# Kernel tuning notes

Hardware: AMD Instinct MI355X
Metric: run time of the kernel (lower is better)

Reference implementation:

```python
import jax, jax.numpy as jnp
import numpy as np

B, S, D = 32, 512, 512          # batch, max splits, HIDDEN_SIZE
H2 = D // 2                      # bidirectional GRU hidden per direction = 256
HEADS = 8
ATT_H = 512                      # ML_ATT_HIDDEN
DK = ATT_H // HEADS
LN_EPS = 1e-5


def setup_inputs() -> dict:
    key = jax.random.key(0)
    ks = jax.random.split(key, 20)
    n = lambda k, shp, s=0.05: jax.random.normal(k, shp, dtype=jnp.float32) * s
    lengths = jax.random.randint(ks[0], (B,), 1, S + 1)
    masks = (jnp.arange(S)[None, :] < lengths[:, None]).astype(jnp.int32)
    return {
        "splits": n(ks[1], (B, S, D), 1.0),
        "w_ih_f": n(ks[2], (3 * H2, D)), "w_hh_f": n(ks[3], (3 * H2, H2)),
        "b_ih_f": n(ks[4], (3 * H2,)), "b_hh_f": n(ks[5], (3 * H2,)),
        "w_ih_b": n(ks[6], (3 * H2, D)), "w_hh_b": n(ks[7], (3 * H2, H2)),
        "b_ih_b": n(ks[8], (3 * H2,)), "b_hh_b": n(ks[9], (3 * H2,)),
        "ln1_g": jnp.ones((D,), jnp.float32), "ln1_b": jnp.zeros((D,), jnp.float32),
        "wq": n(ks[10], (ATT_H, D)), "bq": n(ks[11], (ATT_H,)),
        "wk": n(ks[12], (ATT_H, D)), "bk": n(ks[13], (ATT_H,)),
        "wv": n(ks[14], (ATT_H, D)), "bv": n(ks[15], (ATT_H,)),
        "wo": n(ks[16], (D, ATT_H)), "bo": n(ks[17], (D,)),
        "ln2_g": jnp.ones((D,), jnp.float32), "ln2_b": jnp.zeros((D,), jnp.float32),
        "lengths": lengths, "masks": masks,
    }


def _gru_dir(x, m, w_ih, w_hh, b_ih, b_hh):
    """x: (B,S,D) float, m: (B,S) float {0,1}. Masked GRU, packed-sequence semantics:
    hidden frozen past length, outputs zero at pads, returns (outputs (B,S,H2), h_final (B,H2))."""
    xg = jnp.einsum('bsd,gd->bsg', x, w_ih) + b_ih   # precompute input gates (B,S,3H2)
    xg_t = xg.transpose(1, 0, 2)                      # (S,B,3H2)
    m_t = m.T[:, :, None]                             # (S,B,1)
    h0 = jnp.zeros((x.shape[0], w_hh.shape[1]), x.dtype)

    def step(h, inp):
        xg_s, m_s = inp
        hg = h @ w_hh.T + b_hh
        xr, xz, xn = jnp.split(xg_s, 3, -1)
        hr, hz, hn = jnp.split(hg, 3, -1)
        r = jax.nn.sigmoid(xr + hr)
        z = jax.nn.sigmoid(xz + hz)
        ncand = jnp.tanh(xn + r * hn)
        h_new = (1.0 - z) * ncand + z * h
        h = m_s * h_new + (1.0 - m_s) * h
        return h, h * m_s

    hT, ys = jax.lax.scan(step, h0, (xg_t, m_t))
    return ys.transpose(1, 0, 2), hT


def _layernorm(x, g, b):
    mu = x.mean(-1, keepdims=True)
    var = ((x - mu) ** 2).mean(-1, keepdims=True)
    return (x - mu) / jnp.sqrt(var + LN_EPS) * g + b


def reference(splits, w_ih_f, w_hh_f, b_ih_f, b_hh_f, w_ih_b, w_hh_b, b_ih_b, b_hh_b,
              ln1_g, ln1_b, wq, bq, wk, bk, wv, bv, wo, bo, ln2_g, ln2_b,
              lengths, masks):
    mf = masks.astype(splits.dtype)  # (B,S)
    # bidirectional masked GRU (split_rnn)
    out_f, h_f = _gru_dir(splits, mf, w_ih_f, w_hh_f, b_ih_f, b_hh_f)
    out_b_rev, h_b = _gru_dir(splits[:, ::-1], mf[:, ::-1], w_ih_b, w_hh_b, b_ih_b, b_hh_b)
    outputs = jnp.concatenate([out_f, out_b_rev[:, ::-1]], -1)  # (B,S,D)
    hidden = jnp.concatenate([h_f, h_b], -1)                    # (B,D)
    zm = (lengths != 0).astype(outputs.dtype)
    outputs = outputs * zm[:, None, None]
    hidden = hidden * zm[:, None]
    # split_rnn_norm (LAYER_NORM_USE)
    outputs = _layernorm(outputs, ln1_g, ln1_b)
    # CONTEXT_ATT: masked multi-head self-attention
    m3 = mf[:, None, :] * mf[:, :, None]        # (B,S,S)
    bsz = outputs.shape[0]

    def proj(x, w, b):
        return (x @ w.T + b).reshape(bsz, -1, HEADS, DK).transpose(0, 2, 1, 3)

    q = proj(outputs, wq, bq)
    k = proj(outputs, wk, bk)
    v = proj(outputs, wv, bv)
    scores = jnp.einsum('bhqd,bhkd->bhqk', q, k) / np.sqrt(DK).astype(outputs.dtype)
    mask4 = m3[:, None, :, :]
    scores = jnp.where(mask4 == 0, jnp.asarray(-1e8, scores.dtype), scores)
    p = jax.nn.softmax(scores, axis=-1) * mask4
    attn = jnp.einsum('bhqk,bhkd->bhqd', p, v)
    concat = attn.transpose(0, 2, 1, 3).reshape(bsz, -1, HEADS * DK)
    o = concat @ wo.T + bo
    rowmask = (m3.sum(-1, keepdims=True) > 0).astype(o.dtype)   # (B,S,1)
    o = o * rowmask
    # residual + attn_norm
    outputs = _layernorm(outputs + o, ln2_g, ln2_b)
    return outputs, hidden
```

## Files before the change

kernel.cpp:

```cpp
#include <hip/hip_runtime.h>
#include <hip/hip_bf16.h>
#include <hip/hip_fp16.h>


typedef __bf16 bf16_t;
typedef _Float16 f16_t;
typedef __bf16 bf16x8 __attribute__((ext_vector_type(8)));
typedef __bf16 bf16x4 __attribute__((ext_vector_type(4)));
typedef _Float16 f16x8 __attribute__((ext_vector_type(8)));
typedef float f32x4 __attribute__((ext_vector_type(4)));

#define NB 32
#define NS 512
#define ND 512
#define NH 8
#define DKq 64
#define CH 16

static __device__ __forceinline__ float sigm(float x){ return 1.0f/(1.0f+__expf(-x)); }
static __device__ __forceinline__ float tanh_fast(float x){ return 1.0f - 2.0f/(__expf(2.0f*x)+1.0f); }

__global__ void cvt_f32_bf16_k(const float* __restrict__ src, bf16_t* __restrict__ dst, int n4){
    int i = blockIdx.x*256 + threadIdx.x;
    if (i < n4){
        float4 v = ((const float4*)src)[i];
        bf16x4 o; o[0]=(bf16_t)v.x; o[1]=(bf16_t)v.y; o[2]=(bf16_t)v.z; o[3]=(bf16_t)v.w;
        ((bf16x4*)dst)[i] = o;
    }
}

template<int MODE>
__global__ __launch_bounds__(256,2) void gemm_k(
    const bf16_t* __restrict__ A, const bf16_t* __restrict__ W,
    const float* __restrict__ bias, void* __restrict__ out, void* __restrict__ out2,
    const int* __restrict__ masks, int N)
{
    const int lane = threadIdx.x & 63;
    const int wv = threadIdx.x >> 6;
    const int wr = wv >> 1, wc = wv & 1;
    const int m0 = blockIdx.y*128 + wr*64;
    const int n0 = blockIdx.x*128 + wc*64;
    const int r16 = lane & 15, kq = lane >> 4;
    f32x4 acc[4][4] = {};
    const bf16_t* Ap = A + (size_t)(m0 + r16)*512 + kq*8;
    const bf16_t* Wp = W + (size_t)(n0 + r16)*512 + kq*8;
    #pragma unroll
    for (int kk = 0; kk < 16; ++kk){
        bf16x8 a[4], b[4];
        #pragma unroll
        for (int i=0;i<4;++i) a[i] = *(const bf16x8*)(Ap + (size_t)i*16*512 + kk*32);
        #pragma unroll
        for (int j=0;j<4;++j) b[j] = *(const bf16x8*)(Wp + (size_t)j*16*512 + kk*32);
        #pragma unroll
        for (int i=0;i<4;++i)
            #pragma unroll
            for (int j=0;j<4;++j)
                acc[i][j] = __builtin_amdgcn_mfma_f32_16x16x32_bf16(a[i], b[j], acc[i][j], 0,0,0);
    }
    #pragma unroll
    for (int i=0;i<4;++i){
        int row_base = m0 + i*16 + kq*4;
        #pragma unroll
        for (int j=0;j<4;++j){
            int col = n0 + j*16 + r16;
            float bs = bias[col];
            #pragma unroll
            for (int r=0;r<4;++r){
                int row = row_base + r;
                float v = acc[i][j][r] + bs;
                if (MODE==0){
                    if (col < 768) ((f16_t*)out)[(size_t)row*768 + col] = (f16_t)v;
                    else           ((f16_t*)out2)[(size_t)row*768 + (col-768)] = (f16_t)v;
                } else if (MODE==1){
                    int which = col >> 9, hh = (col >> 6) & 7, d = col & 63;
                    int bb = row >> 9, s = row & 511;
                    ((bf16_t*)out)[((((size_t)which*NB + bb)*NH + hh)*NS + s)*DKq + d] = (bf16_t)v;
                } else {
                    float mrow = (float)masks[row];
                    ((float*)out)[(size_t)row*N + col] = v * mrow;
                }
            }
        }
    }
}

__global__ __launch_bounds__(512,2) void gru_scan_k(
    const f16_t* __restrict__ xg_f, const f16_t* __restrict__ xg_b,
    const float* __restrict__ whh_f, const float* __restrict__ whh_b,
    const float* __restrict__ bhh_f, const float* __restrict__ bhh_b,
    const int* __restrict__ lengths,
    f16_t* __restrict__ gout,
    float* __restrict__ hidden)
{
    const int b = blockIdx.x >> 1, dir = blockIdx.x & 1;
    const int tid = threadIdx.x, lane = tid & 63, w = tid >> 6;
    const int r16 = lane & 15, kq = lane >> 4;
    const float* whh = dir ? whh_b : whh_f;
    const float* bhh = dir ? bhh_b : bhh_f;
    const f16_t* xgd = dir ? xg_b : xg_f;
    const int len = lengths[b];

    __shared__ __align__(16) f16_t  xg_lds[2][CH][768];
    __shared__ __align__(16) f16_t  go_lds[CH][256];
    __shared__ __align__(16) bf16_t h_row[2][256];

    ((bf16_t*)h_row)[tid] = (bf16_t)0.0f;

    const int t0 = dir ? (NS - len) : 0;
    const int t_end = dir ? NS : len;
    const int nch = (len + CH - 1) / CH;

    auto issue_chunk = [&](int ci, int buf){
        int base = t0 + ci*CH;
        int jmax = min(CH, t_end - base);
        int pstart = dir ? (NS - base - jmax) : base;
        const char* gp = (const char*)(xgd + ((size_t)b*NS + pstart)*768);
        char* lp = (char*)(&xg_lds[buf][0][0]);
        int bytes = jmax*1536;
        #pragma unroll
        for (int k2=0; k2<3; ++k2){
            int off = (w*3 + k2)*1024;
            if (off < bytes){
                __builtin_amdgcn_global_load_lds(
                    (const __attribute__((address_space(1))) void*)(gp + off + (size_t)lane*16),
                    (__attribute__((address_space(3))) void*)(lp + off), 16, 0, 0);
            }
        }
    };
    issue_chunk(0, 0);

    bf16x8 wf[6][8];
    #pragma unroll
    for (int tt=0; tt<6; ++tt){
        int g = tt >> 1, u = tt & 1;
        int n0 = g*256 + 32*w + u*16;
        const float* wp = whh + (size_t)(n0 + r16)*256 + kq*8;
        #pragma unroll
        for (int kk=0; kk<8; ++kk){
            float4 v0 = *(const float4*)(wp + kk*32);
            float4 v1 = *(const float4*)(wp + kk*32 + 4);
            bf16x8 f;
            f[0]=(bf16_t)v0.x; f[1]=(bf16_t)v0.y; f[2]=(bf16_t)v0.z; f[3]=(bf16_t)v0.w;
            f[4]=(bf16_t)v1.x; f[5]=(bf16_t)v1.y; f[6]=(bf16_t)v1.z; f[7]=(bf16_t)v1.w;
            wf[tt][kk] = f;
        }
    }
    float bhr[2], bhz[2], bhn[2], hreg[2];
    #pragma unroll
    for (int u=0; u<2; ++u){
        int gi = 32*w + 16*u + r16;
        bhr[u] = bhh[gi]; bhz[u] = bhh[256+gi]; bhn[u] = bhh[512+gi];
        hreg[u] = 0.0f;
    }

    int hp = 0;
    for (int ci = 0; ci < nch; ++ci){
        const int cur = ci & 1;
        const int base = t0 + ci*CH;
        const int jmax = min(CH, t_end - base);
        __syncthreads();
        if (ci + 1 < nch) issue_chunk(ci+1, cur^1);
        for (int j = 0; j < jmax; ++j){
            const int xrow = dir ? (jmax-1-j) : j;
            f32x4 acc[6] = {};
            #pragma unroll
            for (int kk=0; kk<8; ++kk){
                bf16x8 a = {};
                if (r16 == 0) a = *(const bf16x8*)(&h_row[hp][kk*32 + kq*8]);
                #pragma unroll
                for (int tt=0; tt<6; ++tt)
                    acc[tt] = __builtin_amdgcn_mfma_f32_16x16x32_bf16(a, wf[tt][kk], acc[tt], 0,0,0);
            }
            if (lane < 16){
                #pragma unroll
                for (int u=0; u<2; ++u){
                    int gi = 32*w + 16*u + r16;
                    float hr = acc[u][0]   + bhr[u];
                    float hz = acc[2+u][0] + bhz[u];
                    float hn = acc[4+u][0] + bhn[u];
                    float xr = (float)xg_lds[cur][xrow][gi];
                    float xz = (float)xg_lds[cur][xrow][256+gi];
                    float xn = (float)xg_lds[cur][xrow][512+gi];
                    float rr = sigm(xr + hr);
                    float z2 = sigm(xz + hz);
                    float nc = tanh_fast(xn + rr*hn);
                    hreg[u] = (1.0f - z2)*nc + z2*hreg[u];
                    go_lds[j][gi]    = (f16_t)hreg[u];
                    h_row[hp^1][gi]  = (bf16_t)hreg[u];
                }
            }
            hp ^= 1;
            __syncthreads();
        }
        {
            int row = tid >> 5, c8 = tid & 31;
            if (row < jmax){
                int t = base + row;
                int pos = dir ? (NS-1-t) : t;
                f16x8 vv = *(const f16x8*)(&go_lds[row][c8*8]);
                *(f16x8*)(gout + ((size_t)b*NS + pos)*512 + dir*256 + c8*8) = vv;
            }
        }
    }
    if (lane < 16){
        #pragma unroll
        for (int u=0; u<2; ++u)
            hidden[(size_t)b*512 + dir*256 + 32*w + 16*u + r16] = hreg[u];
    }
}

template<int PASS>
__global__ __launch_bounds__(256,4) void ln_k(
    const void* __restrict__ src1, const float* __restrict__ src2,
    const float* __restrict__ gg, const float* __restrict__ bb,
    void* __restrict__ dst)
{
    int row = blockIdx.x*4 + (threadIdx.x>>6);
    int lane = threadIdx.x & 63;
    int c0 = lane*8;
    float x[8];
    if (PASS==1){
        f16x8 v = *(const f16x8*)((const f16_t*)src1 + (size_t)row*512 + c0);
        #pragma unroll
        for (int i=0;i<8;++i) x[i] = (float)v[i];
    } else {
        bf16x8 v = *(const bf16x8*)((const bf16_t*)src1 + (size_t)row*512 + c0);
        const float* q = src2 + (size_t)row*512 + c0;
        float4 q0 = *(const float4*)q, q1 = *(const float4*)(q+4);
        x[0]=(float)v[0]+q0.x; x[1]=(float)v[1]+q0.y; x[2]=(float)v[2]+q0.z; x[3]=(float)v[3]+q0.w;
        x[4]=(float)v[4]+q1.x; x[5]=(float)v[5]+q1.y; x[6]=(float)v[6]+q1.z; x[7]=(float)v[7]+q1.w;
    }
    float s=0.f, sq=0.f;
    #pragma unroll
    for (int i=0;i<8;++i){ s += x[i]; sq += x[i]*x[i]; }
    #pragma unroll
    for (int m=1; m<64; m<<=1){ s += __shfl_xor(s, m, 64); sq += __shfl_xor(sq, m, 64); }
    float mu = s * (1.0f/512.0f);
    float var = sq * (1.0f/512.0f) - mu*mu;
    float rs = rsqrtf(var + 1e-5f);
    if (PASS==1){
        bf16x8 o;
        #pragma unroll
        for (int i=0;i<8;++i) o[i] = (bf16_t)((x[i]-mu)*rs*gg[c0+i] + bb[c0+i]);
        *(bf16x8*)((bf16_t*)dst + (size_t)row*512 + c0) = o;
    } else {
        float y[8];
        #pragma unroll
        for (int i=0;i<8;++i) y[i] = (x[i]-mu)*rs*gg[c0+i] + bb[c0+i];
        float* dp = (float*)dst + (size_t)row*512 + c0;
        *(float4*)dp     = make_float4(y[0],y[1],y[2],y[3]);
        *(float4*)(dp+4) = make_float4(y[4],y[5],y[6],y[7]);
    }
}

__global__ __launch_bounds__(256,2) void attn_k(
    const bf16_t* __restrict__ qkv,
    const int* __restrict__ lengths,
    bf16_t* __restrict__ concat)
{
    const int qb = blockIdx.x, hh = blockIdx.y, b = blockIdx.z;
    const int tid = threadIdx.x, lane = tid & 63, w = tid >> 6;
    const int r16 = lane & 15, kq = lane >> 4;
    const int len = lengths[b];
    const size_t bh = ((size_t)b*NH + hh)*NS*DKq;
    const bf16_t* Q = qkv + bh;
    const bf16_t* K = qkv + (size_t)NB*NH*NS*DKq + bh;
    const bf16_t* V = qkv + 2*(size_t)NB*NH*NS*DKq + bh;

    __shared__ __align__(16) bf16_t VT[32][520];
    __shared__ __align__(16) bf16_t P[4][16][40];

    const int q0 = qb*64 + w*16;
    bf16x8 aq[2];
    #pragma unroll
    for (int kk=0; kk<2; ++kk)
        aq[kk] = *(const bf16x8*)(Q + (size_t)(q0+r16)*DKq + kk*32 + kq*8);

    f32x4 sc[32] = {};
    #pragma unroll
    for (int t=0;t<32;++t){
        #pragma unroll
        for (int kk=0;kk<2;++kk){
            bf16x8 bk = *(const bf16x8*)(K + (size_t)(t*16+r16)*DKq + kk*32 + kq*8);
            sc[t] = __builtin_amdgcn_mfma_f32_16x16x32_bf16(aq[kk], bk, sc[t], 0,0,0);
        }
    }
    float mx[4] = {-3e38f,-3e38f,-3e38f,-3e38f};
    #pragma unroll
    for (int t=0;t<32;++t){
        bool valid = (t*16 + r16) < len;
        #pragma unroll
        for (int r=0;r<4;++r){
            float sv = valid ? sc[t][r]*0.125f : -3e38f;
            sc[t][r] = sv;
            mx[r] = fmaxf(mx[r], sv);
        }
    }
    #pragma unroll
    for (int m=1;m<16;m<<=1)
        #pragma unroll
        for (int r=0;r<4;++r) mx[r] = fmaxf(mx[r], __shfl_xor(mx[r], m, 64));
    float sm[4] = {0.f,0.f,0.f,0.f};
    #pragma unroll
    for (int t=0;t<32;++t){
        bool valid = (t*16 + r16) < len;
        #pragma unroll
        for (int r=0;r<4;++r){
            float p = valid ? __expf(sc[t][r] - mx[r]) : 0.0f;
            sc[t][r] = p;
            sm[r] += p;
        }
    }
    #pragma unroll
    for (int m=1;m<16;m<<=1)
        #pragma unroll
        for (int r=0;r<4;++r) sm[r] += __shfl_xor(sm[r], m, 64);
    float rs[4];
    #pragma unroll
    for (int r=0;r<4;++r) rs[r] = sm[r] > 0.f ? 1.0f/sm[r] : 0.0f;

    f32x4 ao[4] = {};
    #pragma unroll
    for (int half=0; half<2; ++half){
        __syncthreads();
        #pragma unroll
        for (int rr=0; rr<2; ++rr){
            int s = tid*2 + rr;
            const bf16_t* vp = V + (size_t)s*DKq + half*32;
            bf16x8 v0 = *(const bf16x8*)(vp);
            bf16x8 v1 = *(const bf16x8*)(vp+8);
            bf16x8 v2 = *(const bf16x8*)(vp+16);
            bf16x8 v3 = *(const bf16x8*)(vp+24);
            #pragma unroll
            for (int d=0; d<8; ++d){
                VT[d][s]=v0[d]; VT[8+d][s]=v1[d]; VT[16+d][s]=v2[d]; VT[24+d][s]=v3[d];
            }
        }
        __syncthreads();
        #pragma unroll
        for (int c=0;c<16;++c){
            #pragma unroll
            for (int tt=0;tt<2;++tt)
                #pragma unroll
                for (int r=0;r<4;++r)
                    P[w][kq*4 + r][tt*16 + r16] = (bf16_t)(sc[2*c+tt][r] * rs[r]);
            bf16x8 pa = *(const bf16x8*)(&P[w][r16][kq*8]);
            #pragma unroll
            for (int jt=0;jt<2;++jt){
                bf16x8 bvv = *(const bf16x8*)(&VT[jt*16 + r16][c*32 + kq*8]);
                ao[half*2+jt] = __builtin_amdgcn_mfma_f32_16x16x32_bf16(pa, bvv, ao[half*2+jt], 0,0,0);
            }
        }
    }
    #pragma unroll
    for (int ht=0; ht<4; ++ht){
        int d = (ht>>1)*32 + ((ht&1)*16) + r16;
        #pragma unroll
        for (int r=0;r<4;++r){
            int s = q0 + kq*4 + r;
            float v = (s < len) ? ao[ht][r] : 0.0f;
            concat[((size_t)b*NS + s)*512 + hh*DKq + d] = (bf16_t)v;
        }
    }
}

extern "C" void kernel_launch(void* const* d_in, const int* in_sizes, int n_in,
                              void* d_out, int out_size, void* d_ws, size_t ws_size,
                              hipStream_t stream){
    (void)in_sizes; (void)n_in; (void)out_size; (void)ws_size;
    const float* splits = (const float*)d_in[0];
    const float* w_ih_f = (const float*)d_in[1];
    const float* w_hh_f = (const float*)d_in[2];
    const float* b_ih_f = (const float*)d_in[3];
    const float* b_hh_f = (const float*)d_in[4];
    const float* w_ih_b = (const float*)d_in[5];
    const float* w_hh_b = (const float*)d_in[6];
    const float* b_ih_b = (const float*)d_in[7];
    const float* b_hh_b = (const float*)d_in[8];
    const float* ln1_g  = (const float*)d_in[9];
    const float* ln1_b  = (const float*)d_in[10];
    const float* wq     = (const float*)d_in[11];
    const float* bq     = (const float*)d_in[12];
    const float* wk     = (const float*)d_in[13];
    const float* bk_    = (const float*)d_in[14];
    const float* wv     = (const float*)d_in[15];
    const float* bv     = (const float*)d_in[16];
    const float* wo     = (const float*)d_in[17];
    const float* bo     = (const float*)d_in[18];
    const float* ln2_g  = (const float*)d_in[19];
    const float* ln2_b  = (const float*)d_in[20];
    const int* lengths  = (const int*)d_in[21];
    const int* masks    = (const int*)d_in[22];

    char* ws = (char*)d_ws;
    bf16_t* splits16 = (bf16_t*)(ws);
    f16_t*  xg_f     = (f16_t*)(ws + ((size_t)16<<20));
    f16_t*  xg_b     = (f16_t*)(ws + ((size_t)40<<20));
    f16_t*  gout     = (f16_t*)(ws + ((size_t)64<<20));
    bf16_t* ln1out   = (bf16_t*)(ws + ((size_t)80<<20));
    bf16_t* wih16    = (bf16_t*)(ws + ((size_t)96<<20));
    bf16_t* wqkv16   = (bf16_t*)(ws + ((size_t)98<<20));
    bf16_t* wo16     = (bf16_t*)(ws + ((size_t)100<<20));
    float*  bih      = (float*)(ws + ((size_t)101<<20));
    float*  bqkv     = (float*)(ws + ((size_t)101<<20) + 8192);
    bf16_t* qkv      = (bf16_t*)xg_f;
    float*  obuf     = (float*)xg_f;
    bf16_t* concat   = (bf16_t*)splits16;

    float* out_f = (float*)d_out;
    float* hid   = out_f + (size_t)NB*NS*ND;

    hipLaunchKernelGGL(cvt_f32_bf16_k, dim3(8192), dim3(256), 0, stream, splits, splits16, 2097152);
    hipLaunchKernelGGL(cvt_f32_bf16_k, dim3(384),  dim3(256), 0, stream, w_ih_f, wih16,          98304);
    hipLaunchKernelGGL(cvt_f32_bf16_k, dim3(384),  dim3(256), 0, stream, w_ih_b, wih16+393216,   98304);
    hipLaunchKernelGGL(cvt_f32_bf16_k, dim3(256),  dim3(256), 0, stream, wq, wqkv16,             65536);
    hipLaunchKernelGGL(cvt_f32_bf16_k, dim3(256),  dim3(256), 0, stream, wk, wqkv16+262144,      65536);
    hipLaunchKernelGGL(cvt_f32_bf16_k, dim3(256),  dim3(256), 0, stream, wv, wqkv16+524288,      65536);
    hipLaunchKernelGGL(cvt_f32_bf16_k, dim3(256),  dim3(256), 0, stream, wo, wo16,               65536);
    hipMemcpyAsync(bih,       b_ih_f, 768*4, hipMemcpyDeviceToDevice, stream);
    hipMemcpyAsync(bih+768,   b_ih_b, 768*4, hipMemcpyDeviceToDevice, stream);
    hipMemcpyAsync(bqkv,      bq,     512*4, hipMemcpyDeviceToDevice, stream);
    hipMemcpyAsync(bqkv+512,  bk_,    512*4, hipMemcpyDeviceToDevice, stream);
    hipMemcpyAsync(bqkv+1024, bv,     512*4, hipMemcpyDeviceToDevice, stream);
    hipMemsetAsync(gout, 0, (size_t)16<<20, stream);

    hipLaunchKernelGGL((gemm_k<0>), dim3(12,128), dim3(256), 0, stream,
                       splits16, wih16, bih, (void*)xg_f, (void*)xg_b, nullptr, 1536);
    hipLaunchKernelGGL(gru_scan_k, dim3(64), dim3(512), 0, stream,
                       xg_f, xg_b, w_hh_f, w_hh_b, b_hh_f, b_hh_b, lengths, gout, hid);
    hipLaunchKernelGGL((ln_k<1>), dim3(4096), dim3(256), 0, stream,
                       (const void*)gout, nullptr, ln1_g, ln1_b, (void*)ln1out);
    hipLaunchKernelGGL((gemm_k<1>), dim3(12,128), dim3(256), 0, stream,
                       ln1out, wqkv16, bqkv, (void*)qkv, nullptr, nullptr, 0);
    hipLaunchKernelGGL(attn_k, dim3(8,8,32), dim3(256), 0, stream, qkv, lengths, concat);
    hipLaunchKernelGGL((gemm_k<2>), dim3(4,128), dim3(256), 0, stream,
                       concat, wo16, bo, (void*)obuf, nullptr, masks, 512);
    hipLaunchKernelGGL((ln_k<2>), dim3(4096), dim3(256), 0, stream,
                       (const void*)ln1out, obuf, ln2_g, ln2_b, (void*)out_f);
}
```

Baseline: 1.178 ms.

## Tune GRU scan chunking, stream outputs directly, swizzle blocks for XCD locality

The GRU scan now uses 32-step chunks and hoists the LDS reads of the input gates ahead of the recurrent MFMAs. It writes hidden outputs straight to global memory instead of staging them through LDS, and replaces __syncthreads with a raw barrier that only waits on LDS traffic. The GEMM and attention kernels remap block indices so that neighbouring work lands on the same XCD for better L2 reuse. The six weight conversion launches are merged into one multi-segment kernel. The risks are scattered 2-byte global stores per step in the serial scan and doubled LDS use, which could reduce occupancy.

```diff
diff --git a/kernel.cpp b/kernel.cpp
--- a/kernel.cpp
+++ b/kernel.cpp
@@ -15,7 +15,7 @@
 #define ND 512
 #define NH 8
 #define DKq 64
-#define CH 16
+#define CH 32
 
 static __device__ __forceinline__ float sigm(float x){ return 1.0f/(1.0f+__expf(-x)); }
 static __device__ __forceinline__ float tanh_fast(float x){ return 1.0f - 2.0f/(__expf(2.0f*x)+1.0f); }
@@ -26,6 +26,18 @@
         float4 v = ((const float4*)src)[i];
         bf16x4 o; o[0]=(bf16_t)v.x; o[1]=(bf16_t)v.y; o[2]=(bf16_t)v.z; o[3]=(bf16_t)v.w;
         ((bf16x4*)dst)[i] = o;
+    }
+}
+
+struct CvtSeg { const float* src; bf16_t* dst; int n4; };
+struct CvtArgs { CvtSeg seg[6]; };
+__global__ void cvt_multi_k(CvtArgs a){
+    CvtSeg s = a.seg[blockIdx.y];
+    int i = blockIdx.x*256 + threadIdx.x;
+    if (i < s.n4){
+        float4 v = ((const float4*)s.src)[i];
+        bf16x4 o; o[0]=(bf16_t)v.x; o[1]=(bf16_t)v.y; o[2]=(bf16_t)v.z; o[3]=(bf16_t)v.w;
+        ((bf16x4*)s.dst)[i] = o;
     }
 }
 
@@ -38,8 +50,13 @@
     const int lane = threadIdx.x & 63;
     const int wv = threadIdx.x >> 6;
     const int wr = wv >> 1, wc = wv & 1;
-    const int m0 = blockIdx.y*128 + wr*64;
-    const int n0 = blockIdx.x*128 + wc*64;
+    const int nx = gridDim.x;
+    int lin = blockIdx.y * nx + blockIdx.x;
+    int xcd = lin & 7, idx = lin >> 3;
+    int yl = idx / nx, xb = idx - yl*nx;
+    int yb = xcd*16 + yl;
+    const int m0 = yb*128 + wr*64;
+    const int n0 = xb*128 + wc*64;
     const int r16 = lane & 15, kq = lane >> 4;
     f32x4 acc[4][4] = {};
     const bf16_t* Ap = A + (size_t)(m0 + r16)*512 + kq*8;
@@ -101,10 +118,9 @@
     const int len = lengths[b];
 
     __shared__ __align__(16) f16_t  xg_lds[2][CH][768];
-    __shared__ __align__(16) f16_t  go_lds[CH][256];
     __shared__ __align__(16) bf16_t h_row[2][256];
 
-    ((bf16_t*)h_row)[tid] = (bf16_t)0.0f;
+    ((bf16_t*)h_row)[tid & 511] = (bf16_t)0.0f;
 
     const int t0 = dir ? (NS - len) : 0;
     const int t_end = dir ? NS : len;
@@ -118,8 +134,8 @@
         char* lp = (char*)(&xg_lds[buf][0][0]);
         int bytes = jmax*1536;
         #pragma unroll
-        for (int k2=0; k2<3; ++k2){
-            int off = (w*3 + k2)*1024;
+        for (int k2=0; k2<6; ++k2){
+            int off = (w*6 + k2)*1024;
             if (off < bytes){
                 __builtin_amdgcn_global_load_lds(
                     (const __attribute__((address_space(1))) void*)(gp + off + (size_t)lane*16),
@@ -162,6 +178,16 @@
         if (ci + 1 < nch) issue_chunk(ci+1, cur^1);
         for (int j = 0; j < jmax; ++j){
             const int xrow = dir ? (jmax-1-j) : j;
+            float xr[2], xz[2], xn[2];
+            if (lane < 16){
+                #pragma unroll
+                for (int u=0; u<2; ++u){
+                    int gi = 32*w + 16*u + r16;
+                    xr[u] = (float)xg_lds[cur][xrow][gi];
+                    xz[u] = (float)xg_lds[cur][xrow][256+gi];
+                    xn[u] = (float)xg_lds[cur][xrow][512+gi];
+                }
+            }
             f32x4 acc[6] = {};
             #pragma unroll
             for (int kk=0; kk<8; ++kk){
@@ -172,34 +198,26 @@
                     acc[tt] = __builtin_amdgcn_mfma_f32_16x16x32_bf16(a, wf[tt][kk], acc[tt], 0,0,0);
             }
             if (lane < 16){
+                int t = base + j;
+                int pos = dir ? (NS-1-t) : t;
                 #pragma unroll
                 for (int u=0; u<2; ++u){
                     int gi = 32*w + 16*u + r16;
                     float hr = acc[u][0]   + bhr[u];
                     float hz = acc[2+u][0] + bhz[u];
                     float hn = acc[4+u][0] + bhn[u];
-                    float xr = (float)xg_lds[cur][xrow][gi];
-                    float xz = (float)xg_lds[cur][xrow][256+gi];
-                    float xn = (float)xg_lds[cur][xrow][512+gi];
-                    float rr = sigm(xr + hr);
-                    float z2 = sigm(xz + hz);
-                    float nc = tanh_fast(xn + rr*hn);
+                    float rr = sigm(xr[u] + hr);
+                    float z2 = sigm(xz[u] + hz);
+                    float nc = tanh_fast(xn[u] + rr*hn);
                     hreg[u] = (1.0f - z2)*nc + z2*hreg[u];
-                    go_lds[j][gi]    = (f16_t)hreg[u];
-                    h_row[hp^1][gi]  = (bf16_t)hreg[u];
+                    h_row[hp^1][gi] = (bf16_t)hreg[u];
+                    gout[((size_t)b*NS + pos)*512 + dir*256 + gi] = (f16_t)hreg[u];
                 }
             }
             hp ^= 1;
-            __syncthreads();
-        }
-        {
-            int row = tid >> 5, c8 = tid & 31;
-            if (row < jmax){
-                int t = base + row;
-                int pos = dir ? (NS-1-t) : t;
-                f16x8 vv = *(const f16x8*)(&go_lds[row][c8*8]);
-                *(f16x8*)(gout + ((size_t)b*NS + pos)*512 + dir*256 + c8*8) = vv;
-            }
+            asm volatile("s_waitcnt lgkmcnt(0)" ::: "memory");
+            __builtin_amdgcn_s_barrier();
+            asm volatile("" ::: "memory");
         }
     }
     if (lane < 16){
@@ -258,14 +276,18 @@
     const int* __restrict__ lengths,
     bf16_t* __restrict__ concat)
 {
-    const int qb = blockIdx.x, hh = blockIdx.y, b = blockIdx.z;
+    int lin = blockIdx.x + 8*(blockIdx.y + 8*blockIdx.z);
+    int xcd = lin & 7, idx = lin >> 3;
+    int qb = idx & 7;
+    int bh = (xcd << 5) | (idx >> 3);
+    int hh = bh & 7, b = bh >> 3;
     const int tid = threadIdx.x, lane = tid & 63, w = tid >> 6;
     const int r16 = lane & 15, kq = lane >> 4;
     const int len = lengths[b];
-    const size_t bh = ((size_t)b*NH + hh)*NS*DKq;
-    const bf16_t* Q = qkv + bh;
-    const bf16_t* K = qkv + (size_t)NB*NH*NS*DKq + bh;
-    const bf16_t* V = qkv + 2*(size_t)NB*NH*NS*DKq + bh;
+    const size_t bhof = ((size_t)b*NH + hh)*NS*DKq;
+    const bf16_t* Q = qkv + bhof;
+    const bf16_t* K = qkv + (size_t)NB*NH*NS*DKq + bhof;
+    const bf16_t* V = qkv + 2*(size_t)NB*NH*NS*DKq + bhof;
 
     __shared__ __align__(16) bf16_t VT[32][520];
     __shared__ __align__(16) bf16_t P[4][16][40];
@@ -411,12 +433,14 @@
     float* hid   = out_f + (size_t)NB*NS*ND;
 
     hipLaunchKernelGGL(cvt_f32_bf16_k, dim3(8192), dim3(256), 0, stream, splits, splits16, 2097152);
-    hipLaunchKernelGGL(cvt_f32_bf16_k, dim3(384),  dim3(256), 0, stream, w_ih_f, wih16,          98304);
-    hipLaunchKernelGGL(cvt_f32_bf16_k, dim3(384),  dim3(256), 0, stream, w_ih_b, wih16+393216,   98304);
-    hipLaunchKernelGGL(cvt_f32_bf16_k, dim3(256),  dim3(256), 0, stream, wq, wqkv16,             65536);
-    hipLaunchKernelGGL(cvt_f32_bf16_k, dim3(256),  dim3(256), 0, stream, wk, wqkv16+262144,      65536);
-    hipLaunchKernelGGL(cvt_f32_bf16_k, dim3(256),  dim3(256), 0, stream, wv, wqkv16+524288,      65536);
-    hipLaunchKernelGGL(cvt_f32_bf16_k, dim3(256),  dim3(256), 0, stream, wo, wo16,               65536);
+    CvtArgs ca;
+    ca.seg[0] = { w_ih_f, wih16,          98304 };
+    ca.seg[1] = { w_ih_b, wih16+393216,   98304 };
+    ca.seg[2] = { wq,     wqkv16,         65536 };
+    ca.seg[3] = { wk,     wqkv16+262144,  65536 };
+    ca.seg[4] = { wv,     wqkv16+524288,  65536 };
+    ca.seg[5] = { wo,     wo16,           65536 };
+    hipLaunchKernelGGL(cvt_multi_k, dim3(384,6), dim3(256), 0, stream, ca);
     hipMemcpyAsync(bih,       b_ih_f, 768*4, hipMemcpyDeviceToDevice, stream);
     hipMemcpyAsync(bih+768,   b_ih_b, 768*4, hipMemcpyDeviceToDevice, stream);
     hipMemcpyAsync(bqkv,      bq,     512*4, hipMemcpyDeviceToDevice, stream);
```

Measured after the change: 1.249 ms. 1.06x slower.
